# Kernel tuning notes

Hardware: AMD Instinct MI355X
Metric: run time of the kernel (lower is better)

Reference implementation:

```python
import jax, jax.numpy as jnp
import numpy as np

K_TOP = 32
TEMPERATURE = 0.1
EPS = 1e-12  # torch F.normalize eps


def _l2_normalize(x):
    n = jnp.linalg.norm(x, axis=-1, keepdims=True)
    return x / jnp.maximum(n, EPS)


def setup_inputs() -> dict:
    key = jax.random.key(0)
    kq, kk, kv = jax.random.split(key, 3)
    B, T, d_k, d_v, N = 4, 512, 512, 512, 65536
    queries = jax.random.normal(kq, (B, T, d_k), dtype=jnp.float32)
    keys = jax.random.normal(kk, (N, d_k), dtype=jnp.float32)
    values = jax.random.normal(kv, (N, d_v), dtype=jnp.float32)
    return {"queries": queries, "keys": keys, "values": values}


def reference(queries, keys, values):
    B, T, d_k = queries.shape
    d_v = values.shape[1]
    flat_q = queries.reshape(B * T, d_k)
    qn = _l2_normalize(flat_q)           # [BT, d_k]
    kn = _l2_normalize(keys)             # [N, d_k]
    scores = qn @ kn.T                   # [BT, N] cosine similarities
    topk_scores, topk_idx = jax.lax.top_k(scores, K_TOP)  # [BT, K]
    attn = jax.nn.softmax(topk_scores / TEMPERATURE, axis=-1)  # [BT, K]
    retrieved = values[topk_idx]         # [BT, K, d_v]
    aggregated = jnp.einsum('nk,nkd->nd', attn, retrieved)  # [BT, d_v]
    return (aggregated.reshape(B, T, d_v),
            attn.reshape(B, T, K_TOP),
            topk_idx.reshape(B, T, K_TOP))
```

## Files before the change

kernel.cpp:

```cpp
#include <hip/hip_runtime.h>
#include <math.h>

#define M_ROWS 2048
#define N_KEYS 65536
#define DKK 512
#define DVV 512
#define KTOP 32
#define NSPLIT 32
#define NRANGE (N_KEYS / NSPLIT)
#define BM 128
#define BN 128
#define NTILES (NRANGE / BN)
#define KSTEPS (DKK / 32)
#define CAP 8

typedef _Float16 f16x8 __attribute__((ext_vector_type(8)));
typedef _Float16 f16x4v __attribute__((ext_vector_type(4)));
typedef float f32x4 __attribute__((ext_vector_type(4)));


__device__ __forceinline__ void split4(const float4 v, float inv,
                                       _Float16* ph, _Float16* pl) {
  f16x4v h, l;
  float y;
  y = v.x * inv; h[0] = (_Float16)y; l[0] = (_Float16)(y - (float)h[0]);
  y = v.y * inv; h[1] = (_Float16)y; l[1] = (_Float16)(y - (float)h[1]);
  y = v.z * inv; h[2] = (_Float16)y; l[2] = (_Float16)(y - (float)h[2]);
  y = v.w * inv; h[3] = (_Float16)y; l[3] = (_Float16)(y - (float)h[3]);
  *(f16x4v*)ph = h; *(f16x4v*)pl = l;
}

__global__ void __launch_bounds__(256) norm_split_kernel(
    const float* __restrict__ q, const float* __restrict__ keys,
    _Float16* __restrict__ Qh, _Float16* __restrict__ Ql,
    _Float16* __restrict__ Kh, _Float16* __restrict__ Kl) {
  const int gw = (blockIdx.x * 256 + threadIdx.x) >> 6;
  const int lane = threadIdx.x & 63;
  const float* row; _Float16 *oh, *ol;
  if (gw < M_ROWS) {
    row = q + (size_t)gw * DKK; oh = Qh + (size_t)gw * DKK; ol = Ql + (size_t)gw * DKK;
  } else {
    const int n = gw - M_ROWS;
    if (n >= N_KEYS) return;
    row = keys + (size_t)n * DKK; oh = Kh + (size_t)n * DKK; ol = Kl + (size_t)n * DKK;
  }
  const float4 a = ((const float4*)row)[lane];
  const float4 b = ((const float4*)row)[lane + 64];
  float s = a.x*a.x + a.y*a.y + a.z*a.z + a.w*a.w
          + b.x*b.x + b.y*b.y + b.z*b.z + b.w*b.w;
#pragma unroll
  for (int off = 32; off; off >>= 1) s += __shfl_xor(s, off);
  const float inv = 1.0f / fmaxf(sqrtf(s), 1e-12f);
  split4(a, inv, oh + lane * 4,       ol + lane * 4);
  split4(b, inv, oh + 256 + lane * 4, ol + 256 + lane * 4);
}

__device__ __forceinline__ void insert32(float* tS, int* tI, float s, int idx) {
  const float ms = tS[31]; const int mi_ = tI[31];
  if (s < ms || (s == ms && idx > mi_)) return;
  int p = 0;
  while (p < KTOP && (tS[p] > s || (tS[p] == s && tI[p] < idx))) ++p;
  for (int qq = KTOP - 1; qq > p; --qq) { tS[qq] = tS[qq-1]; tI[qq] = tI[qq-1]; }
  tS[p] = s; tI[p] = idx;
}

#define LOADREGS(B, NN, KOF) do {                                        \
  const size_t _q0 = qa0 + (size_t)(KOF), _q1 = qa1 + (size_t)(KOF);     \
  const size_t _k0 = (size_t)(NN) * DKK + ka0 + (size_t)(KOF);           \
  const size_t _k1 = (size_t)(NN) * DKK + ka1 + (size_t)(KOF);           \
  B[0] = *(const f16x8*)&Qh[_q0]; B[1] = *(const f16x8*)&Ql[_q0];        \
  B[2] = *(const f16x8*)&Kh[_k0]; B[3] = *(const f16x8*)&Kl[_k0];        \
  B[4] = *(const f16x8*)&Qh[_q1]; B[5] = *(const f16x8*)&Ql[_q1];        \
  B[6] = *(const f16x8*)&Kh[_k1]; B[7] = *(const f16x8*)&Kl[_k1];        \
} while (0)

#define WRITELDS(B) do {                                                 \
  *(f16x8*)&stAh[sw0] = B[0]; *(f16x8*)&stAl[sw0] = B[1];                \
  *(f16x8*)&stBh[sw0] = B[2]; *(f16x8*)&stBl[sw0] = B[3];                \
  *(f16x8*)&stAh[sw1] = B[4]; *(f16x8*)&stAl[sw1] = B[5];                \
  *(f16x8*)&stBh[sw1] = B[6]; *(f16x8*)&stBl[sw1] = B[7];                \
} while (0)

__global__ void __launch_bounds__(256, 2) gemm_topk_kernel(
    const _Float16* __restrict__ Qh, const _Float16* __restrict__ Ql,
    const _Float16* __restrict__ Kh, const _Float16* __restrict__ Kl,
    float* __restrict__ pscore, int* __restrict__ pidx) {
  __shared__ __attribute__((aligned(16))) _Float16 stAh[BM*32], stAl[BM*32], stBh[BN*32], stBl[BN*32];
  __shared__ float topS[128*33];
  __shared__ int   topI[128*33];
  __shared__ float candS[128*9];
  __shared__ int   candI[128*9];
  __shared__ float mS[128];
  __shared__ int   cnt[128];
  __shared__ int   sOver;

  const int tid  = threadIdx.x;
  const int lane = tid & 63;
  const int w    = tid >> 6;
  const int wr   = w >> 1, wc = w & 1;
  const int cl   = lane & 15;
  const int g    = lane >> 4;
  const int g4   = g * 4;

  const int lin   = (int)(blockIdx.x + gridDim.x * blockIdx.y);
  const int virt  = (lin & 7) * 64 + (lin >> 3);
  const int mblk  = virt & 15;
  const int split = virt >> 4;
  const int qbase  = mblk * BM;
  const int nbase0 = split * NRANGE;

  const int r0 = tid >> 2, o0 = tid & 3;
  const int r1 = r0 + 64;
  const size_t qa0 = (size_t)(qbase + r0) * DKK + o0 * 8;
  const size_t qa1 = qa0 + (size_t)64 * DKK;
  const size_t ka0 = (size_t)r0 * DKK + o0 * 8;
  const size_t ka1 = ka0 + (size_t)64 * DKK;
  const int sw0 = r0 * 32 + 8 * (o0 ^ ((r0 >> 1) & 3));
  const int sw1 = r1 * 32 + 8 * (o0 ^ ((r1 >> 1) & 3));

  int swA[4], swB[4];
#pragma unroll
  for (int mi = 0; mi < 4; ++mi) {
    const int r = wr * 64 + mi * 16 + cl;
    swA[mi] = r * 32 + 8 * (g ^ ((r >> 1) & 3));
  }
#pragma unroll
  for (int ni = 0; ni < 4; ++ni) {
    const int c = wc * 64 + ni * 16 + cl;
    swB[ni] = c * 32 + 8 * (g ^ ((c >> 1) & 3));
  }

  if (tid < 128) {
    mS[tid] = -INFINITY; cnt[tid] = 0;
#pragma unroll
    for (int j = 0; j < KTOP; ++j) { topS[tid*33+j] = -INFINITY; topI[tid*33+j] = 0x7fffffff; }
  }
  if (tid == 0) sOver = 0;
  __syncthreads();

  f16x8 bufA[8], bufB[8];
  LOADREGS(bufA, nbase0, 0);

  for (int ct = 0; ct < NTILES; ++ct) {
    const int n0 = nbase0 + ct * BN;
    f32x4 acc[4][4];
#pragma unroll
    for (int mi = 0; mi < 4; ++mi)
#pragma unroll
      for (int ni = 0; ni < 4; ++ni) acc[mi][ni] = (f32x4)0.0f;

#pragma unroll
    for (int ks = 0; ks < KSTEPS; ++ks) {
      __syncthreads();
      if ((ks & 1) == 0) WRITELDS(bufA); else WRITELDS(bufB);
      __syncthreads();

      if (ks < KSTEPS - 1) {
        if ((ks & 1) == 0) { LOADREGS(bufB, n0, (ks + 1) * 32); }
        else               { LOADREGS(bufA, n0, (ks + 1) * 32); }
      } else if (ct + 1 < NTILES) {
        LOADREGS(bufA, n0 + BN, 0);
      }

      f16x8 Ah[4], Al[4], Bh[4], Bl[4];
#pragma unroll
      for (int mi = 0; mi < 4; ++mi) {
        Ah[mi] = *(const f16x8*)&stAh[swA[mi]];
        Al[mi] = *(const f16x8*)&stAl[swA[mi]];
      }
#pragma unroll
      for (int ni = 0; ni < 4; ++ni) {
        Bh[ni] = *(const f16x8*)&stBh[swB[ni]];
        Bl[ni] = *(const f16x8*)&stBl[swB[ni]];
      }
#pragma unroll
      for (int mi = 0; mi < 4; ++mi)
#pragma unroll
        for (int ni = 0; ni < 4; ++ni) {
          acc[mi][ni] = __builtin_amdgcn_mfma_f32_16x16x32_f16(Al[mi], Bh[ni], acc[mi][ni], 0, 0, 0);
          acc[mi][ni] = __builtin_amdgcn_mfma_f32_16x16x32_f16(Ah[mi], Bl[ni], acc[mi][ni], 0, 0, 0);
          acc[mi][ni] = __builtin_amdgcn_mfma_f32_16x16x32_f16(Ah[mi], Bh[ni], acc[mi][ni], 0, 0, 0);
        }
    }

    float m[4][4];
#pragma unroll
    for (int mi = 0; mi < 4; ++mi) {
      const f32x4 mv = *(const f32x4*)&mS[wr * 64 + mi * 16 + g4];
      m[mi][0] = mv[0]; m[mi][1] = mv[1]; m[mi][2] = mv[2]; m[mi][3] = mv[3];
    }
    unsigned long long pend = 0ull;
#pragma unroll
    for (int mi = 0; mi < 4; ++mi)
#pragma unroll
      for (int ni = 0; ni < 4; ++ni)
#pragma unroll
        for (int j = 0; j < 4; ++j)
          if (acc[mi][ni][j] >= m[mi][j])
            pend |= 1ull << (mi * 16 + ni * 4 + j);

    for (;;) {
      if (pend) {
#pragma unroll
        for (int mi = 0; mi < 4; ++mi)
#pragma unroll
          for (int ni = 0; ni < 4; ++ni)
#pragma unroll
            for (int j = 0; j < 4; ++j) {
              const int bit = mi * 16 + ni * 4 + j;
              if (pend & (1ull << bit)) {
                const int r = wr * 64 + mi * 16 + g4 + j;
                const int t = atomicAdd(&cnt[r], 1);
                if (t < CAP) {
                  candS[r * 9 + t] = acc[mi][ni][j];
                  candI[r * 9 + t] = n0 + wc * 64 + ni * 16 + cl;
                  pend &= ~(1ull << bit);
                }
              }
            }
      }
      __syncthreads();
      if (tid < 128) {
        int nc = cnt[tid];
        if (nc > CAP) { sOver = 1; nc = CAP; }
        float* tS = &topS[tid * 33];
        int*   tI = &topI[tid * 33];
        for (int e = 0; e < nc; ++e) insert32(tS, tI, candS[tid * 9 + e], candI[tid * 9 + e]);
        mS[tid] = tS[KTOP - 1];
        cnt[tid] = 0;
      }
      __syncthreads();
      const int over = sOver;
      __syncthreads();
      if (tid == 0) sOver = 0;
      if (!over) break;
#pragma unroll
      for (int mi = 0; mi < 4; ++mi) {
        const f32x4 mv = *(const f32x4*)&mS[wr * 64 + mi * 16 + g4];
        m[mi][0] = mv[0]; m[mi][1] = mv[1]; m[mi][2] = mv[2]; m[mi][3] = mv[3];
      }
      unsigned long long keep = 0ull;
#pragma unroll
      for (int mi = 0; mi < 4; ++mi)
#pragma unroll
        for (int ni = 0; ni < 4; ++ni)
#pragma unroll
          for (int j = 0; j < 4; ++j) {
            const int bit = mi * 16 + ni * 4 + j;
            if ((pend & (1ull << bit)) && acc[mi][ni][j] >= m[mi][j])
              keep |= 1ull << bit;
          }
      pend = keep;
    }
  }

  if (tid < 128) {
    const size_t base = ((size_t)(qbase + tid) * NSPLIT + split) * KTOP;
    for (int j = 0; j < KTOP; ++j) {
      pscore[base + j] = topS[tid * 33 + j];
      pidx[base + j]   = topI[tid * 33 + j];
    }
  }
}


#define QB 128
#define NB 128
#define KC 32
#define FNTILES (NRANGE / NB)
#define KCH (DKK / KC)
#define LDST 132

__global__ void __launch_bounds__(256) norm_kernel(
    const float* __restrict__ q, const float* __restrict__ keys,
    float* __restrict__ qn, float* __restrict__ kinv) {
  const int gw = (blockIdx.x * 256 + threadIdx.x) >> 6;
  const int lane = threadIdx.x & 63;
  if (gw < M_ROWS) {
    const float* row = q + (size_t)gw * DKK;
    float4 a = ((const float4*)row)[lane];
    float4 b = ((const float4*)row)[lane + 64];
    float s = a.x*a.x + a.y*a.y + a.z*a.z + a.w*a.w
            + b.x*b.x + b.y*b.y + b.z*b.z + b.w*b.w;
#pragma unroll
    for (int off = 32; off; off >>= 1) s += __shfl_xor(s, off);
    const float inv = 1.0f / fmaxf(sqrtf(s), 1e-12f);
    float* orow = qn + (size_t)gw * DKK;
    ((float4*)orow)[lane]      = make_float4(a.x*inv, a.y*inv, a.z*inv, a.w*inv);
    ((float4*)orow)[lane + 64] = make_float4(b.x*inv, b.y*inv, b.z*inv, b.w*inv);
  } else {
    const int n = gw - M_ROWS;
    if (n < N_KEYS) {
      const float* row = keys + (size_t)n * DKK;
      float4 a = ((const float4*)row)[lane];
      float4 b = ((const float4*)row)[lane + 64];
      float s = a.x*a.x + a.y*a.y + a.z*a.z + a.w*a.w
              + b.x*b.x + b.y*b.y + b.z*b.z + b.w*b.w;
#pragma unroll
      for (int off = 32; off; off >>= 1) s += __shfl_xor(s, off);
      if (lane == 0) kinv[n] = 1.0f / fmaxf(sqrtf(s), 1e-12f);
    }
  }
}

__device__ __forceinline__ void lds_wr_tile(float* dst, int k8, int r, float4 v, float scale) {
  dst[(k8 * 4 + 0) * LDST + r] = v.x * scale;
  dst[(k8 * 4 + 1) * LDST + r] = v.y * scale;
  dst[(k8 * 4 + 2) * LDST + r] = v.z * scale;
  dst[(k8 * 4 + 3) * LDST + r] = v.w * scale;
}

__global__ void __launch_bounds__(256, 1) score_topk_kernel(
    const float* __restrict__ qn, const float* __restrict__ keys,
    const float* __restrict__ kinv,
    float* __restrict__ pscore, int* __restrict__ pidx) {
  __shared__ float u[16896];
  __shared__ float topS[QB * KTOP];
  __shared__ int   topI[QB * KTOP];

  const int tid = threadIdx.x;
  const int tx = tid & 15, ty = tid >> 4;
  const int qbase = blockIdx.y * QB;
  const int nbase0 = blockIdx.x * NRANGE;

  for (int i = tid; i < QB * KTOP; i += 256) { topS[i] = -INFINITY; topI[i] = 0; }
  __syncthreads();

  for (int t = 0; t < FNTILES; ++t) {
    const int n0 = nbase0 + t * NB;
    float acc[8][8];
#pragma unroll
    for (int i = 0; i < 8; ++i)
#pragma unroll
      for (int j = 0; j < 8; ++j) acc[i][j] = 0.0f;

#pragma unroll
    for (int p = 0; p < 4; ++p) {
      const int id = tid + p * 256;
      const int r = id >> 3, k8 = id & 7;
      const float4 va = *(const float4*)&qn[(size_t)(qbase + r) * DKK + k8 * 4];
      const float4 vb = *(const float4*)&keys[(size_t)(n0 + r) * DKK + k8 * 4];
      const float kv = kinv[n0 + r];
      lds_wr_tile(u, k8, r, va, 1.0f);
      lds_wr_tile(u + 4224, k8, r, vb, kv);
    }
    __syncthreads();

    for (int kc = 0; kc < KCH; ++kc) {
      float4 pa[4], pb[4]; float pk[4];
      const bool pre = (kc + 1 < KCH);
      if (pre) {
#pragma unroll
        for (int p = 0; p < 4; ++p) {
          const int id = tid + p * 256;
          const int r = id >> 3, k8 = id & 7;
          pa[p] = *(const float4*)&qn[(size_t)(qbase + r) * DKK + (kc + 1) * KC + k8 * 4];
          pb[p] = *(const float4*)&keys[(size_t)(n0 + r) * DKK + (kc + 1) * KC + k8 * 4];
          pk[p] = kinv[n0 + r];
        }
      }
      const float* As = u + (kc & 1) * 8448;
      const float* Bs = As + 4224;
#pragma unroll 4
      for (int kk = 0; kk < KC; ++kk) {
        const float4 a0 = *(const float4*)&As[kk * LDST + ty * 4];
        const float4 a1 = *(const float4*)&As[kk * LDST + ty * 4 + 64];
        const float4 b0 = *(const float4*)&Bs[kk * LDST + tx * 4];
        const float4 b1 = *(const float4*)&Bs[kk * LDST + tx * 4 + 64];
        const float av[8] = {a0.x,a0.y,a0.z,a0.w,a1.x,a1.y,a1.z,a1.w};
        const float bv[8] = {b0.x,b0.y,b0.z,b0.w,b1.x,b1.y,b1.z,b1.w};
#pragma unroll
        for (int i = 0; i < 8; ++i)
#pragma unroll
          for (int j = 0; j < 8; ++j)
            acc[i][j] = fmaf(av[i], bv[j], acc[i][j]);
      }
      if (pre) {
        float* Ad = u + ((kc + 1) & 1) * 8448;
        float* Bd = Ad + 4224;
#pragma unroll
        for (int p = 0; p < 4; ++p) {
          const int id = tid + p * 256;
          const int r = id >> 3, k8 = id & 7;
          lds_wr_tile(Ad, k8, r, pa[p], 1.0f);
          lds_wr_tile(Bd, k8, r, pb[p], pk[p]);
        }
      }
      __syncthreads();
    }

#pragma unroll
    for (int ib = 0; ib < 2; ++ib)
#pragma unroll
      for (int i = 0; i < 4; ++i) {
        const int r = ty * 4 + i + ib * 64;
#pragma unroll
        for (int jb = 0; jb < 2; ++jb) {
          *(float4*)&u[r * LDST + tx * 4 + jb * 64] =
              make_float4(acc[ib*4+i][jb*4+0], acc[ib*4+i][jb*4+1],
                          acc[ib*4+i][jb*4+2], acc[ib*4+i][jb*4+3]);
        }
      }
    __syncthreads();

    if (tid < QB) {
      const int row = tid;
      float* tS = &topS[row * KTOP];
      int*   tI = &topI[row * KTOP];
      float mSv = tS[KTOP - 1]; int mIv = tI[KTOP - 1];
      for (int c4 = 0; c4 < NB / 4; ++c4) {
        const float4 v = *(const float4*)&u[row * LDST + c4 * 4];
#pragma unroll
        for (int wv = 0; wv < 4; ++wv) {
          const float s = (&v.x)[wv];
          const int idx = n0 + c4 * 4 + wv;
          if (s > mSv || (s == mSv && idx < mIv)) {
            int p = 0;
            while (p < KTOP && (tS[p] > s || (tS[p] == s && tI[p] < idx))) ++p;
            for (int qq = KTOP - 1; qq > p; --qq) { tS[qq] = tS[qq-1]; tI[qq] = tI[qq-1]; }
            tS[p] = s; tI[p] = idx;
            mSv = tS[KTOP - 1]; mIv = tI[KTOP - 1];
          }
        }
      }
    }
    __syncthreads();
  }

  if (tid < QB) {
    const size_t base = ((size_t)(qbase + tid) * NSPLIT + blockIdx.x) * KTOP;
    for (int j = 0; j < KTOP; ++j) {
      pscore[base + j] = topS[tid * KTOP + j];
      pidx[base + j]   = topI[tid * KTOP + j];
    }
  }
}

__global__ void __launch_bounds__(256) merge_kernel(
    const float* __restrict__ pscore, const int* __restrict__ pidx,
    const float* __restrict__ values,
    float* __restrict__ out_agg, float* __restrict__ out_attn, float* __restrict__ out_idx) {
  __shared__ float attn_s[KTOP];
  __shared__ int   sel_i[KTOP];
  const int row = blockIdx.x;
  const int tid = threadIdx.x;

  if (tid < 64) {
    const int lane = tid;
    const float* ps = pscore + (size_t)row * NSPLIT * KTOP;
    const int*   pi = pidx   + (size_t)row * NSPLIT * KTOP;
    int pos = 0;
    float s; int idx;
    if (lane < NSPLIT) { s = ps[lane * KTOP]; idx = pi[lane * KTOP]; }
    else { s = -INFINITY; idx = 0x7fffffff; }
    for (int it = 0; it < KTOP; ++it) {
      float wsv = s; int wi = idx; int wl = lane;
#pragma unroll
      for (int off = 32; off; off >>= 1) {
        const float os = __shfl_xor(wsv, off);
        const int   oi = __shfl_xor(wi, off);
        const int   ol = __shfl_xor(wl, off);
        if (os > wsv || (os == wsv && oi < wi)) { wsv = os; wi = oi; wl = ol; }
      }
      if (lane == 0) { attn_s[it] = wsv; sel_i[it] = wi; }
      if (lane == wl) {
        ++pos;
        if (pos < KTOP) { s = ps[lane * KTOP + pos]; idx = pi[lane * KTOP + pos]; }
        else { s = -INFINITY; idx = 0x7fffffff; }
      }
    }
  }
  __syncthreads();
  if (tid < KTOP) {
    const float mm = attn_s[0];
    const float e = expf((attn_s[tid] - mm) * 10.0f);
    float tsum = e;
#pragma unroll
    for (int off = 16; off; off >>= 1) tsum += __shfl_xor(tsum, off);
    const float a = e / tsum;
    out_attn[(size_t)row * KTOP + tid] = a;
    out_idx [(size_t)row * KTOP + tid] = (float)sel_i[tid];
    attn_s[tid] = a;
  }
  __syncthreads();

  const int d = tid * 2;
  float2 accv = make_float2(0.0f, 0.0f);
  for (int j = 0; j < KTOP; ++j) {
    const float wgt = attn_s[j];
    const float2 v = *(const float2*)&values[(size_t)sel_i[j] * DVV + d];
    accv.x = fmaf(wgt, v.x, accv.x);
    accv.y = fmaf(wgt, v.y, accv.y);
  }
  *(float2*)&out_agg[(size_t)row * DVV + d] = accv;
}

extern "C" void kernel_launch(void* const* d_in, const int* in_sizes, int n_in,
                              void* d_out, int out_size, void* d_ws, size_t ws_size,
                              hipStream_t stream) {
  const float* q      = (const float*)d_in[0];
  const float* keys   = (const float*)d_in[1];
  const float* values = (const float*)d_in[2];

  float* out      = (float*)d_out;
  float* out_agg  = out;
  float* out_attn = out + (size_t)M_ROWS * DVV;
  float* out_idx  = out_attn + (size_t)M_ROWS * KTOP;

  const size_t needFast =
      (size_t)M_ROWS * DKK * 2 * 2
    + (size_t)N_KEYS * DKK * 2 * 2
    + (size_t)M_ROWS * NSPLIT * KTOP * 8;

  if (ws_size >= needFast) {
    _Float16* Qh = (_Float16*)d_ws;
    _Float16* Ql = Qh + (size_t)M_ROWS * DKK;
    _Float16* Kh = Ql + (size_t)M_ROWS * DKK;
    _Float16* Kl = Kh + (size_t)N_KEYS * DKK;
    float* pscore = (float*)(Kl + (size_t)N_KEYS * DKK);
    int*   pidx   = (int*)(pscore + (size_t)M_ROWS * NSPLIT * KTOP);

    norm_split_kernel<<<(M_ROWS + N_KEYS) / 4, 256, 0, stream>>>(q, keys, Qh, Ql, Kh, Kl);
    dim3 g2(M_ROWS / BM, NSPLIT, 1);
    gemm_topk_kernel<<<g2, 256, 0, stream>>>(Qh, Ql, Kh, Kl, pscore, pidx);
    merge_kernel<<<M_ROWS, 256, 0, stream>>>(pscore, pidx, values, out_agg, out_attn, out_idx);
  } else {
    float* ws     = (float*)d_ws;
    float* qn     = ws;
    float* kinv   = qn + (size_t)M_ROWS * DKK;
    float* pscore = kinv + N_KEYS;
    int*   pidx   = (int*)(pscore + (size_t)M_ROWS * NSPLIT * KTOP);

    norm_kernel<<<(M_ROWS + N_KEYS) / 4, 256, 0, stream>>>(q, keys, qn, kinv);
    dim3 g2(NSPLIT, M_ROWS / QB, 1);
    score_topk_kernel<<<g2, 256, 0, stream>>>(qn, keys, kinv, pscore, pidx);
    merge_kernel<<<M_ROWS, 256, 0, stream>>>(pscore, pidx, values, out_agg, out_attn, out_idx);
  }
}
```

Baseline: 1.865 ms.

## Stream K tiles via global_load_lds double buffer, read Q directly from global

Replaces the register-staged double buffer for both Q and K with direct global-to-LDS loads (global_load_lds) into a two-slot LDS ring for the K hi/lo tiles, cutting per-k-step syncs from two to one. Q fragments are now loaded straight from global memory into registers each k-step instead of going through LDS, relying on cache reuse. The candidate capacity per row grows from 8 to 12 to reduce overflow retry passes in the top-k merge. This frees VGPRs and LDS write instructions but adds uncoalesced global Q traffic per step and depends on correct LDS swizzle and synchronization of async loads.

```diff
diff --git a/kernel.cpp b/kernel.cpp
--- a/kernel.cpp
+++ b/kernel.cpp
@@ -12,7 +12,8 @@
 #define BN 128
 #define NTILES (NRANGE / BN)
 #define KSTEPS (DKK / 32)
-#define CAP 8
+#define CAP 12
+#define CSTR 13
 
 typedef _Float16 f16x8 __attribute__((ext_vector_type(8)));
 typedef _Float16 f16x4v __attribute__((ext_vector_type(4)));
@@ -64,32 +65,55 @@
   tS[p] = s; tI[p] = idx;
 }
 
-#define LOADREGS(B, NN, KOF) do {                                        \
-  const size_t _q0 = qa0 + (size_t)(KOF), _q1 = qa1 + (size_t)(KOF);     \
-  const size_t _k0 = (size_t)(NN) * DKK + ka0 + (size_t)(KOF);           \
-  const size_t _k1 = (size_t)(NN) * DKK + ka1 + (size_t)(KOF);           \
-  B[0] = *(const f16x8*)&Qh[_q0]; B[1] = *(const f16x8*)&Ql[_q0];        \
-  B[2] = *(const f16x8*)&Kh[_k0]; B[3] = *(const f16x8*)&Kl[_k0];        \
-  B[4] = *(const f16x8*)&Qh[_q1]; B[5] = *(const f16x8*)&Ql[_q1];        \
-  B[6] = *(const f16x8*)&Kh[_k1]; B[7] = *(const f16x8*)&Kl[_k1];        \
+#define GLL4(BUFV, NNBASE, KOF) do {                                           \
+  const size_t _kb = (size_t)(NNBASE) * DKK + (size_t)(KOF);                   \
+  __builtin_amdgcn_global_load_lds(                                            \
+    (const __attribute__((address_space(1))) void*)(Kh + _kb + boff0),         \
+    (__attribute__((address_space(3))) void*)&stB[(BUFV)*8192 + bld0], 16, 0, 0); \
+  __builtin_amdgcn_global_load_lds(                                            \
+    (const __attribute__((address_space(1))) void*)(Kh + _kb + boff1),         \
+    (__attribute__((address_space(3))) void*)&stB[(BUFV)*8192 + bld1], 16, 0, 0); \
+  __builtin_amdgcn_global_load_lds(                                            \
+    (const __attribute__((address_space(1))) void*)(Kl + _kb + boff0),         \
+    (__attribute__((address_space(3))) void*)&stB[(BUFV)*8192 + 4096 + bld0], 16, 0, 0); \
+  __builtin_amdgcn_global_load_lds(                                            \
+    (const __attribute__((address_space(1))) void*)(Kl + _kb + boff1),         \
+    (__attribute__((address_space(3))) void*)&stB[(BUFV)*8192 + 4096 + bld1], 16, 0, 0); \
 } while (0)
 
-#define WRITELDS(B) do {                                                 \
-  *(f16x8*)&stAh[sw0] = B[0]; *(f16x8*)&stAl[sw0] = B[1];                \
-  *(f16x8*)&stBh[sw0] = B[2]; *(f16x8*)&stBl[sw0] = B[3];                \
-  *(f16x8*)&stAh[sw1] = B[4]; *(f16x8*)&stAl[sw1] = B[5];                \
-  *(f16x8*)&stBh[sw1] = B[6]; *(f16x8*)&stBl[sw1] = B[7];                \
+#define KSTEP(KS, BUF, NXT, PN0, PKOF, DOPREF) do {                            \
+  __syncthreads();                                                             \
+  f16x8 Bh_[4], Bl_[4], Ah_[4], Al_[4];                                        \
+  _Pragma("unroll")                                                            \
+  for (int ni = 0; ni < 4; ++ni) {                                             \
+    Bh_[ni] = *(const f16x8*)&stB[(BUF)*8192 + swB[ni]];                       \
+    Bl_[ni] = *(const f16x8*)&stB[(BUF)*8192 + 4096 + swB[ni]];                \
+  }                                                                            \
+  _Pragma("unroll")                                                            \
+  for (int mi = 0; mi < 4; ++mi) {                                             \
+    Ah_[mi] = *(const f16x8*)&Qh[aoff[mi] + (KS)*32];                          \
+    Al_[mi] = *(const f16x8*)&Ql[aoff[mi] + (KS)*32];                          \
+  }                                                                            \
+  if (DOPREF) { GLL4(NXT, PN0, PKOF); }                                        \
+  _Pragma("unroll")                                                            \
+  for (int mi = 0; mi < 4; ++mi)                                               \
+    _Pragma("unroll")                                                          \
+    for (int ni = 0; ni < 4; ++ni) {                                           \
+      acc[mi][ni] = __builtin_amdgcn_mfma_f32_16x16x32_f16(Al_[mi], Bh_[ni], acc[mi][ni], 0, 0, 0); \
+      acc[mi][ni] = __builtin_amdgcn_mfma_f32_16x16x32_f16(Ah_[mi], Bl_[ni], acc[mi][ni], 0, 0, 0); \
+      acc[mi][ni] = __builtin_amdgcn_mfma_f32_16x16x32_f16(Ah_[mi], Bh_[ni], acc[mi][ni], 0, 0, 0); \
+    }                                                                          \
 } while (0)
 
 __global__ void __launch_bounds__(256, 2) gemm_topk_kernel(
     const _Float16* __restrict__ Qh, const _Float16* __restrict__ Ql,
     const _Float16* __restrict__ Kh, const _Float16* __restrict__ Kl,
     float* __restrict__ pscore, int* __restrict__ pidx) {
-  __shared__ __attribute__((aligned(16))) _Float16 stAh[BM*32], stAl[BM*32], stBh[BN*32], stBl[BN*32];
-  __shared__ float topS[128*33];
-  __shared__ int   topI[128*33];
-  __shared__ float candS[128*9];
-  __shared__ int   candI[128*9];
+  __shared__ __attribute__((aligned(16))) _Float16 stB[2 * 2 * BN * 32];
+  __shared__ float topS[128 * 33];
+  __shared__ int   topI[128 * 33];
+  __shared__ float candS[128 * CSTR];
+  __shared__ int   candI[128 * CSTR];
   __shared__ float mS[128];
   __shared__ int   cnt[128];
   __shared__ int   sOver;
@@ -109,21 +133,19 @@
   const int qbase  = mblk * BM;
   const int nbase0 = split * NRANGE;
 
-  const int r0 = tid >> 2, o0 = tid & 3;
-  const int r1 = r0 + 64;
-  const size_t qa0 = (size_t)(qbase + r0) * DKK + o0 * 8;
-  const size_t qa1 = qa0 + (size_t)64 * DKK;
-  const size_t ka0 = (size_t)r0 * DKK + o0 * 8;
-  const size_t ka1 = ka0 + (size_t)64 * DKK;
-  const int sw0 = r0 * 32 + 8 * (o0 ^ ((r0 >> 1) & 3));
-  const int sw1 = r1 * 32 + 8 * (o0 ^ ((r1 >> 1) & 3));
-
-  int swA[4], swB[4];
-#pragma unroll
-  for (int mi = 0; mi < 4; ++mi) {
-    const int r = wr * 64 + mi * 16 + cl;
-    swA[mi] = r * 32 + 8 * (g ^ ((r >> 1) & 3));
-  }
+  size_t aoff[4];
+#pragma unroll
+  for (int mi = 0; mi < 4; ++mi)
+    aoff[mi] = (size_t)(qbase + wr * 64 + mi * 16 + cl) * DKK + g * 8;
+
+  const int c0 = (w * 2 + 0) * 16 + (lane >> 2);
+  const int c1 = (w * 2 + 1) * 16 + (lane >> 2);
+  const size_t boff0 = (size_t)c0 * DKK + (size_t)((((lane & 3) ^ ((c0 >> 1) & 3)) * 8));
+  const size_t boff1 = (size_t)c1 * DKK + (size_t)((((lane & 3) ^ ((c1 >> 1) & 3)) * 8));
+  const int bld0 = __builtin_amdgcn_readfirstlane((w * 2 + 0) * 512);
+  const int bld1 = __builtin_amdgcn_readfirstlane((w * 2 + 1) * 512);
+
+  int swB[4];
 #pragma unroll
   for (int ni = 0; ni < 4; ++ni) {
     const int c = wc * 64 + ni * 16 + cl;
@@ -138,8 +160,7 @@
   if (tid == 0) sOver = 0;
   __syncthreads();
 
-  f16x8 bufA[8], bufB[8];
-  LOADREGS(bufA, nbase0, 0);
+  GLL4(0, nbase0, 0);
 
   for (int ct = 0; ct < NTILES; ++ct) {
     const int n0 = nbase0 + ct * BN;
@@ -150,37 +171,13 @@
       for (int ni = 0; ni < 4; ++ni) acc[mi][ni] = (f32x4)0.0f;
 
 #pragma unroll
-    for (int ks = 0; ks < KSTEPS; ++ks) {
-      __syncthreads();
-      if ((ks & 1) == 0) WRITELDS(bufA); else WRITELDS(bufB);
-      __syncthreads();
-
-      if (ks < KSTEPS - 1) {
-        if ((ks & 1) == 0) { LOADREGS(bufB, n0, (ks + 1) * 32); }
-        else               { LOADREGS(bufA, n0, (ks + 1) * 32); }
-      } else if (ct + 1 < NTILES) {
-        LOADREGS(bufA, n0 + BN, 0);
-      }
-
-      f16x8 Ah[4], Al[4], Bh[4], Bl[4];
-#pragma unroll
-      for (int mi = 0; mi < 4; ++mi) {
-        Ah[mi] = *(const f16x8*)&stAh[swA[mi]];
-        Al[mi] = *(const f16x8*)&stAl[swA[mi]];
-      }
-#pragma unroll
-      for (int ni = 0; ni < 4; ++ni) {
-        Bh[ni] = *(const f16x8*)&stBh[swB[ni]];
-        Bl[ni] = *(const f16x8*)&stBl[swB[ni]];
-      }
-#pragma unroll
-      for (int mi = 0; mi < 4; ++mi)
-#pragma unroll
-        for (int ni = 0; ni < 4; ++ni) {
-          acc[mi][ni] = __builtin_amdgcn_mfma_f32_16x16x32_f16(Al[mi], Bh[ni], acc[mi][ni], 0, 0, 0);
-          acc[mi][ni] = __builtin_amdgcn_mfma_f32_16x16x32_f16(Ah[mi], Bl[ni], acc[mi][ni], 0, 0, 0);
-          acc[mi][ni] = __builtin_amdgcn_mfma_f32_16x16x32_f16(Ah[mi], Bh[ni], acc[mi][ni], 0, 0, 0);
-        }
+    for (int ks2 = 0; ks2 < 8; ++ks2) {
+      KSTEP(ks2 * 2, 0, 1, n0, (ks2 * 2 + 1) * 32, 1);
+      if (ks2 < 7) {
+        KSTEP(ks2 * 2 + 1, 1, 0, n0, (ks2 * 2 + 2) * 32, 1);
+      } else {
+        KSTEP(15, 1, 0, n0 + BN, 0, (ct + 1 < NTILES));
+      }
     }
 
     float m[4][4];
@@ -212,8 +209,8 @@
                 const int r = wr * 64 + mi * 16 + g4 + j;
                 const int t = atomicAdd(&cnt[r], 1);
                 if (t < CAP) {
-                  candS[r * 9 + t] = acc[mi][ni][j];
-                  candI[r * 9 + t] = n0 + wc * 64 + ni * 16 + cl;
+                  candS[r * CSTR + t] = acc[mi][ni][j];
+                  candI[r * CSTR + t] = n0 + wc * 64 + ni * 16 + cl;
                   pend &= ~(1ull << bit);
                 }
               }
@@ -225,7 +222,7 @@
         if (nc > CAP) { sOver = 1; nc = CAP; }
         float* tS = &topS[tid * 33];
         int*   tI = &topI[tid * 33];
-        for (int e = 0; e < nc; ++e) insert32(tS, tI, candS[tid * 9 + e], candI[tid * 9 + e]);
+        for (int e = 0; e < nc; ++e) insert32(tS, tI, candS[tid * CSTR + e], candI[tid * CSTR + e]);
         mS[tid] = tS[KTOP - 1];
         cnt[tid] = 0;
       }
```

Result: slower. 2.033 ms (+9.0%).
